# Kernel tuning notes

Measured on AMD Instinct MI355X. Metric: run time of the kernel, lower is better.

## Reference

```python
import jax, jax.numpy as jnp
import numpy as np

N_NODES = 20000
N_EDGES = 320000
NF = 128   # num_node_feats
EF = 32    # num_edge_feats
CF = 3     # num_coord_feats
H = 512    # hidden_dim


def setup_inputs() -> dict:
    key = jax.random.key(0)
    ks = jax.random.split(key, 20)
    s = lambda k, shape, fan_in: jax.random.normal(k, shape, jnp.float32) / np.sqrt(fan_in)
    return {
        "hfeats": jax.random.normal(ks[0], (N_NODES, NF), jnp.float32),
        "cfeats": jax.random.normal(ks[1], (N_NODES, CF), jnp.float32),
        "efeats": jax.random.normal(ks[2], (N_EDGES, EF), jnp.float32),
        "src": jax.random.randint(ks[3], (N_EDGES,), 0, N_NODES, jnp.int32),
        "dst": jax.random.randint(ks[4], (N_EDGES,), 0, N_NODES, jnp.int32),
        # node_expansion: Linear(NF, H)
        "Wn": s(ks[5], (NF, H), NF), "bn": jnp.zeros((H,), jnp.float32),
        # edge_expansion: Linear(EF, H)
        "We": s(ks[6], (EF, H), EF), "be": jnp.zeros((H,), jnp.float32),
        # coord_expansion: Linear(CF, H)
        "Wc": s(ks[7], (CF, H), CF), "bc": jnp.zeros((H,), jnp.float32),
        # combination_reduction_nfeats: Linear(H,H) -> CELU -> Linear(H,NF) -> CELU
        "Wn1": s(ks[8], (H, H), H), "bn1": jnp.zeros((H,), jnp.float32),
        "Wn2": s(ks[9], (H, NF), H), "bn2": jnp.zeros((NF,), jnp.float32),
        # combination_reduction_efeats: Linear(H, EF) -> CELU
        "Weo": s(ks[10], (H, EF), H), "beo": jnp.zeros((EF,), jnp.float32),
        # combination_reduction_cfeats: Linear(H, CF) -> CELU
        "Wco": s(ks[11], (H, CF), H), "bco": jnp.zeros((CF,), jnp.float32),
    }


def reference(hfeats, cfeats, efeats, src, dst,
              Wn, bn, We, be, Wc, bc,
              Wn1, bn1, Wn2, bn2, Weo, beo, Wco, bco):
    celu = jax.nn.celu
    n_nodes = hfeats.shape[0]
    # Feature expansions (Linear + CELU)
    h = celu(hfeats @ Wn + bn)   # [N, H]
    e = celu(efeats @ We + be)   # [E, H]
    c = celu(cfeats @ Wc + bc)   # [N, H]
    # edge_udf: x = |c_dst - c_src| * (h_src * e)   -> [E, H]
    x = jnp.abs(c[dst] - c[src]) * (h[src] * e)
    # update_all(copy_e, sum): scatter-sum edge messages to dst nodes
    k = jax.ops.segment_sum(x, dst, num_segments=n_nodes)  # [N, H]
    # Residual combination-reductions
    h_out = hfeats + celu(celu(k @ Wn1 + bn1) @ Wn2 + bn2)
    e_out = efeats + celu(e @ Weo + beo)
    c_out = cfeats + celu(c @ Wco + bco)
    return (h_out, c_out, e_out)
```

## Files before the change

kernel.cpp:

```cpp
#include <hip/hip_runtime.h>
#include <hip/hip_bf16.h>

#define NF 128
#define EF 32
#define CF 3
#define H  512
#define EB 32

typedef __attribute__((ext_vector_type(8))) short bf16x8;
typedef __attribute__((ext_vector_type(4))) float f32x4;

__device__ __forceinline__ float celu_f(float x) {
    return fmaxf(x, __expf(fminf(x, 0.0f)) - 1.0f);
}
__device__ __forceinline__ uint cvtpk(float lo, float hi) {
    uint r;
    asm("v_cvt_pk_bf16_f32 %0, %1, %2" : "=v"(r) : "v"(lo), "v"(hi));
    return r;
}
__device__ __forceinline__ bf16x8 pack8(float4 v0, float4 v1) {
    union { uint4 u; bf16x8 b; } r;
    r.u.x = cvtpk(v0.x, v0.y); r.u.y = cvtpk(v0.z, v0.w);
    r.u.z = cvtpk(v1.x, v1.y); r.u.w = cvtpk(v1.z, v1.w);
    return r.b;
}
__device__ __forceinline__ float b2f(ushort s) {
    union { uint u; float f; } v; v.u = ((uint)s) << 16; return v.f;
}
__device__ __forceinline__ void unpack4(uint2 v, float* o) {
    union { uint u; float f; } x;
    x.u = v.x << 16;          o[0] = x.f;
    x.u = v.x & 0xffff0000u;  o[1] = x.f;
    x.u = v.y << 16;          o[2] = x.f;
    x.u = v.y & 0xffff0000u;  o[3] = x.f;
}

__global__ void hist_kernel(const int* __restrict__ dst, int* __restrict__ cnt, int n_edges) {
    int i = blockIdx.x * 256 + threadIdx.x;
    if (i < n_edges) atomicAdd(&cnt[dst[i]], 1);
}

__global__ void scan_kernel(int* __restrict__ cnt, int n_nodes) {
    __shared__ int part[1024];
    const int t = threadIdx.x;
    const int per = (n_nodes + 1023) / 1024;
    int s = 0;
    for (int i = 0; i < per; ++i) {
        int idx = t * per + i;
        if (idx < n_nodes) s += cnt[idx];
    }
    part[t] = s;
    __syncthreads();
    for (int off = 1; off < 1024; off <<= 1) {
        int v = (t >= off) ? part[t - off] : 0;
        __syncthreads();
        part[t] += v;
        __syncthreads();
    }
    int acc = part[t] - s;
    for (int i = 0; i < per; ++i) {
        int idx = t * per + i;
        if (idx < n_nodes) {
            int c = cnt[idx];
            cnt[idx] = acc;
            acc += c;
        }
    }
}

__global__ void scatter_kernel(const int* __restrict__ dst, int* __restrict__ cursor,
                               int* __restrict__ perm, int n_edges) {
    int i = blockIdx.x * 256 + threadIdx.x;
    if (i < n_edges) {
        int pos = atomicAdd(&cursor[dst[i]], 1);
        perm[pos] = i;
    }
}

__global__ void prep_kernel(const float* __restrict__ We, const float* __restrict__ Weo,
                            const float* __restrict__ Wn, const float* __restrict__ Wn1,
                            const float* __restrict__ Wn2,
                            ushort* __restrict__ Wet, ushort* __restrict__ Weot,
                            ushort* __restrict__ Wnt, ushort* __restrict__ Wn1t,
                            ushort* __restrict__ Wn2t) {
    int i = blockIdx.x * 256 + threadIdx.x;
    if (i < H * EF) {
        int j = i / EF, k = i % EF;
        Wet[i] = (ushort)cvtpk(We[(size_t)k * H + j], 0.f);
        int o = i / H, j2 = i % H;
        Weot[i] = (ushort)cvtpk(Weo[(size_t)j2 * EF + o], 0.f);
    }
    if (i < H * NF) {
        int o = i >> 7, k = i & 127;
        Wnt[i] = (ushort)cvtpk(Wn[(size_t)k * H + o], 0.f);
        int o2 = i >> 9, k2 = i & 511;
        Wn2t[i] = (ushort)cvtpk(Wn2[(size_t)k2 * NF + o2], 0.f);
    }
    if (i < H * H) {
        int o = i >> 9, k = i & 511;
        Wn1t[i] = (ushort)cvtpk(Wn1[(size_t)k * H + o], 0.f);
    }
}

__global__ __launch_bounds__(256) void node_expand_kernel(
        const float* __restrict__ hfeats, const float* __restrict__ cfeats,
        const ushort* __restrict__ Wnt, const float* __restrict__ bn,
        const float* __restrict__ Wc, const float* __restrict__ bc,
        ushort* __restrict__ hc, int n_nodes) {
    __shared__ ushort hf[32 * NF];
    __shared__ float cf[32][4];
    const int t = threadIdx.x;
    const int lane = t & 63;
    const int w = t >> 6;
    const int node0 = blockIdx.x * 32;

    for (int i = t; i < 32 * 16; i += 256) {
        int row = i >> 4, g = i & 15;
        int node = node0 + row; if (node >= n_nodes) node = n_nodes - 1;
        const float* p = hfeats + (size_t)node * NF + g * 8;
        float4 v0 = *(const float4*)p;
        float4 v1 = *(const float4*)(p + 4);
        ((bf16x8*)hf)[row * 16 + (g ^ (row & 7))] = pack8(v0, v1);
    }
    for (int i = t; i < 32 * CF; i += 256) {
        int n = i / CF, k = i % CF;
        int node = node0 + n; if (node >= n_nodes) node = n_nodes - 1;
        cf[n][k] = cfeats[(size_t)node * CF + k];
    }
    __syncthreads();

    const int ar = lane & 15;
    const int hi = lane >> 4;
    const int ak = hi * 8;

    f32x4 acc[2][8];
    #pragma unroll
    for (int nt = 0; nt < 2; ++nt)
        #pragma unroll
        for (int q = 0; q < 8; ++q) { f32x4 z = {0.f,0.f,0.f,0.f}; acc[nt][q] = z; }

    for (int kstep = 0; kstep < NF / 32; ++kstep) {
        bf16x8 nfrag[2];
        #pragma unroll
        for (int nt = 0; nt < 2; ++nt) {
            int r = nt * 16 + ar;
            int g = kstep * 4 + hi;
            nfrag[nt] = ((const bf16x8*)hf)[r * 16 + (g ^ (r & 7))];
        }
        #pragma unroll
        for (int q = 0; q < 8; ++q) {
            bf16x8 wf = *(const bf16x8*)(Wnt + (size_t)((w * 8 + q) * 16 + ar) * NF + kstep * 32 + ak);
            acc[0][q] = __builtin_amdgcn_mfma_f32_16x16x32_bf16(wf, nfrag[0], acc[0][q], 0, 0, 0);
            acc[1][q] = __builtin_amdgcn_mfma_f32_16x16x32_bf16(wf, nfrag[1], acc[1][q], 0, 0, 0);
        }
    }
    #pragma unroll
    for (int q = 0; q < 8; ++q) {
        const int jbase = (w * 8 + q) * 16 + hi * 4;
        const float4 bv = *(const float4*)(bn + jbase);
        #pragma unroll
        for (int nt = 0; nt < 2; ++nt) {
            int node = node0 + nt * 16 + ar;
            if (node < n_nodes) {
                uint2 pk;
                pk.x = cvtpk(celu_f(acc[nt][q][0] + bv.x), celu_f(acc[nt][q][1] + bv.y));
                pk.y = cvtpk(celu_f(acc[nt][q][2] + bv.z), celu_f(acc[nt][q][3] + bv.w));
                *(uint2*)(hc + (size_t)node * 1024 + (jbase >> 2) * 8) = pk;
            }
        }
    }

    for (int i = t; i < 32 * 64; i += 256) {
        int n = i >> 6, gj = i & 63;
        int node = node0 + n;
        if (node < n_nodes) {
            int j = gj * 8;
            float c0 = cf[n][0], c1 = cf[n][1], c2 = cf[n][2];
            float v[8];
            #pragma unroll
            for (int u = 0; u < 8; ++u)
                v[u] = celu_f(bc[j + u] + c0 * Wc[j + u] + c1 * Wc[H + j + u] + c2 * Wc[2 * H + j + u]);
            uint2 p0, p1;
            p0.x = cvtpk(v[0], v[1]); p0.y = cvtpk(v[2], v[3]);
            p1.x = cvtpk(v[4], v[5]); p1.y = cvtpk(v[6], v[7]);
            *(uint2*)(hc + (size_t)node * 1024 + (2 * gj) * 8 + 4) = p0;
            *(uint2*)(hc + (size_t)node * 1024 + (2 * gj + 1) * 8 + 4) = p1;
        }
    }
}

__global__ __launch_bounds__(256) void c_out_kernel(
        const float* __restrict__ cfeats, const ushort* __restrict__ hc,
        const float* __restrict__ Wco, const float* __restrict__ bco,
        float* __restrict__ c_out, int n_nodes) {
    const int t = threadIdx.x;
    const int lane = t & 63;
    const int w = t >> 6;
    const int node = blockIdx.x * 4 + w;
    if (node >= n_nodes) return;
    uint2 cv0 = *(const uint2*)(hc + (size_t)node * 1024 + (2 * lane) * 8 + 4);
    uint2 cv1 = *(const uint2*)(hc + (size_t)node * 1024 + (2 * lane + 1) * 8 + 4);
    float cv[8];
    unpack4(cv0, cv);
    unpack4(cv1, cv + 4);
    float a0 = 0.f, a1 = 0.f, a2 = 0.f;
    #pragma unroll
    for (int u = 0; u < 8; ++u) {
        int j = lane * 8 + u;
        a0 += cv[u] * Wco[j * CF + 0];
        a1 += cv[u] * Wco[j * CF + 1];
        a2 += cv[u] * Wco[j * CF + 2];
    }
    #pragma unroll
    for (int m = 32; m >= 1; m >>= 1) {
        a0 += __shfl_xor(a0, m);
        a1 += __shfl_xor(a1, m);
        a2 += __shfl_xor(a2, m);
    }
    if (lane < 3) {
        float s = (lane == 0) ? a0 : (lane == 1) ? a1 : a2;
        c_out[(size_t)node * CF + lane] = cfeats[(size_t)node * CF + lane] + celu_f(bco[lane] + s);
    }
}

__global__ __launch_bounds__(512, 4) void edge_kernel(
        const float* __restrict__ efeats,
        const int* __restrict__ src, const int* __restrict__ dst,
        const int* __restrict__ perm,
        const ushort* __restrict__ Wet, const float* __restrict__ be,
        const ushort* __restrict__ Weot, const float* __restrict__ beo,
        const ushort* __restrict__ hc,
        float* __restrict__ k_acc, float* __restrict__ e_out, int n_edges) {
    __shared__ ushort e512[EB * 512];
    __shared__ int s_perm[EB], s_src[EB], s_dst[EB];
    const int t = threadIdx.x;
    const int lane = t & 63;
    const int w = t >> 6;

    const int nwg = gridDim.x;
    const int q = nwg >> 3, r = nwg & 7;
    const int xcd = blockIdx.x & 7, sub = blockIdx.x >> 3;
    const int bid = (xcd < r ? xcd * (q + 1) : r * (q + 1) + (xcd - r) * q) + sub;
    const int e0 = bid * EB;

    if (t < EB) {
        int e = e0 + t;
        int pe = (e < n_edges) ? perm[e] : -1;
        s_perm[t] = pe;
        s_src[t] = (pe >= 0) ? src[pe] : 0;
        s_dst[t] = (pe >= 0) ? dst[pe] : -1;
    }
    __syncthreads();

    const int ar = lane & 15;
    const int hi = lane >> 4;
    const int ak = hi * 8;

    {
        bf16x8 wfrag[4];
        #pragma unroll
        for (int qq = 0; qq < 4; ++qq)
            wfrag[qq] = *(const bf16x8*)(Wet + (size_t)((w * 4 + qq) * 16 + ar) * EF + ak);
        #pragma unroll
        for (int et = 0; et < 2; ++et) {
            bf16x8 efrag;
            {
                int pe = s_perm[et * 16 + ar];
                if (pe < 0) pe = 0;
                const float* p = efeats + (size_t)pe * EF + ak;
                float4 v0 = *(const float4*)p;
                float4 v1 = *(const float4*)(p + 4);
                efrag = pack8(v0, v1);
            }
            f32x4 acc[4];
            #pragma unroll
            for (int qq = 0; qq < 4; ++qq) { f32x4 z = {0.f,0.f,0.f,0.f}; acc[qq] = z; }
            #pragma unroll
            for (int qq = 0; qq < 4; ++qq)
                acc[qq] = __builtin_amdgcn_mfma_f32_16x16x32_bf16(wfrag[qq], efrag, acc[qq], 0, 0, 0);
            const int e_l = et * 16 + ar;
            #pragma unroll
            for (int qq = 0; qq < 4; ++qq) {
                const int jbase = (w * 4 + qq) * 16 + hi * 4;
                const float4 bv = *(const float4*)(be + jbase);
                uint2 pk;
                pk.x = cvtpk(celu_f(acc[qq][0] + bv.x), celu_f(acc[qq][1] + bv.y));
                pk.y = cvtpk(celu_f(acc[qq][2] + bv.z), celu_f(acc[qq][3] + bv.w));
                const int gs = (jbase >> 3) ^ (e_l & 7);
                *(uint2*)(&e512[e_l * 512 + gs * 8 + (jbase & 7)]) = pk;
            }
        }
    }
    __syncthreads();

    if (w < 4) {
        const int grp = t >> 7;
        const int ct = t & 127;
        const int j0 = ct * 4;
        const int g = j0 >> 3, go = j0 & 7;
        const int ebase = grp * 16;
        float a_[4];
        a_[0] = a_[1] = a_[2] = a_[3] = 0.f;
        int cur = -1;

        uint4 svb[2][4];
        uint2 cdb[2][4];
        uint2 evb[2][4];

        #pragma unroll
        for (int j = 0; j < 4; ++j) {
            const int e = ebase + j;
            const int s_ = s_src[e];
            int dc = s_dst[e]; dc = (dc < 0) ? 0 : dc;
            svb[0][j] = *(const uint4*)(hc + (size_t)s_ * 1024 + ct * 8);
            cdb[0][j] = *(const uint2*)(hc + (size_t)dc * 1024 + ct * 8 + 4);
            evb[0][j] = *(const uint2*)(&e512[e * 512 + (g ^ (e & 7)) * 8 + go]);
        }

        #pragma unroll
        for (int c = 0; c < 4; ++c) {
            const int cb = c & 1, nb = cb ^ 1;
            if (c < 3) {
                #pragma unroll
                for (int j = 0; j < 4; ++j) {
                    const int e = ebase + (c + 1) * 4 + j;
                    const int s_ = s_src[e];
                    int dc = s_dst[e]; dc = (dc < 0) ? 0 : dc;
                    svb[nb][j] = *(const uint4*)(hc + (size_t)s_ * 1024 + ct * 8);
                    cdb[nb][j] = *(const uint2*)(hc + (size_t)dc * 1024 + ct * 8 + 4);
                    evb[nb][j] = *(const uint2*)(&e512[e * 512 + (g ^ (e & 7)) * 8 + go]);
                }
            }
            #pragma unroll
            for (int j = 0; j < 4; ++j) {
                const int e = ebase + c * 4 + j;
                const int d = __builtin_amdgcn_readfirstlane(s_dst[e]);
                if (d != cur) {
                    if (cur >= 0) {
                        #pragma unroll
                        for (int u = 0; u < 4; ++u)
                            atomicAdd(&k_acc[(size_t)cur * H + j0 + u], a_[u]);
                        a_[0] = a_[1] = a_[2] = a_[3] = 0.f;
                    }
                    cur = d;
                }
                if (d >= 0) {
                    float hs_[4], cs_[4], cd_[4], ev_[4];
                    uint2 hv; hv.x = svb[cb][j].x; hv.y = svb[cb][j].y;
                    uint2 cv; cv.x = svb[cb][j].z; cv.y = svb[cb][j].w;
                    unpack4(hv, hs_);
                    unpack4(cv, cs_);
                    unpack4(cdb[cb][j], cd_);
                    unpack4(evb[cb][j], ev_);
                    #pragma unroll
                    for (int u = 0; u < 4; ++u)
                        a_[u] += fabsf(cd_[u] - cs_[u]) * (hs_[u] * ev_[u]);
                }
            }
        }
        if (cur >= 0) {
            #pragma unroll
            for (int u = 0; u < 4; ++u)
                atomicAdd(&k_acc[(size_t)cur * H + j0 + u], a_[u]);
        }
    } else {
        const int wc = w - 4;
        const int ot = wc & 1, et = wc >> 1;
        const int e_l = et * 16 + ar;
        f32x4 accc = {0.f, 0.f, 0.f, 0.f};
        #pragma unroll
        for (int kt = 0; kt < 16; ++kt) {
            bf16x8 wfC = *(const bf16x8*)(Weot + (size_t)(ot * 16 + ar) * H + kt * 32 + ak);
            const int gs = (kt * 4 + hi) ^ (e_l & 7);
            bf16x8 b = *(const bf16x8*)(&e512[e_l * 512 + gs * 8]);
            accc = __builtin_amdgcn_mfma_f32_16x16x32_bf16(wfC, b, accc, 0, 0, 0);
        }
        const int pe = s_perm[e_l];
        if (pe >= 0) {
            const int obase = ot * 16 + hi * 4;
            const float4 bo = *(const float4*)(beo + obase);
            size_t idx = (size_t)pe * EF + obase;
            float4 ef4 = *(const float4*)(efeats + idx);
            float4 o;
            o.x = ef4.x + celu_f(accc[0] + bo.x);
            o.y = ef4.y + celu_f(accc[1] + bo.y);
            o.z = ef4.z + celu_f(accc[2] + bo.z);
            o.w = ef4.w + celu_f(accc[3] + bo.w);
            *(float4*)(e_out + idx) = o;
        }
    }
}

__global__ __launch_bounds__(256) void node_out_kernel(
        const float* __restrict__ hfeats, const float* __restrict__ k_acc,
        const ushort* __restrict__ Wn1t, const float* __restrict__ bn1,
        const ushort* __restrict__ Wn2t, const float* __restrict__ bn2,
        float* __restrict__ h_out, int n_nodes) {
    __shared__ ushort kt_s[32 * H];
    const int t = threadIdx.x;
    const int lane = t & 63;
    const int w = t >> 6;
    const int node0 = blockIdx.x * 32;

    for (int i = t; i < 32 * 64; i += 256) {
        int row = i >> 6, g = i & 63;
        int node = node0 + row; if (node >= n_nodes) node = n_nodes - 1;
        const float* p = k_acc + (size_t)node * H + g * 8;
        float4 v0 = *(const float4*)p;
        float4 v1 = *(const float4*)(p + 4);
        ((bf16x8*)kt_s)[row * 64 + (g ^ (row & 7))] = pack8(v0, v1);
    }
    __syncthreads();

    const int ar = lane & 15;
    const int hi = lane >> 4;
    const int ak = hi * 8;

    f32x4 acc[2][8];
    #pragma unroll
    for (int nt = 0; nt < 2; ++nt)
        #pragma unroll
        for (int q = 0; q < 8; ++q) { f32x4 z = {0.f,0.f,0.f,0.f}; acc[nt][q] = z; }

    for (int kstep = 0; kstep < H / 32; ++kstep) {
        bf16x8 kfrag[2];
        #pragma unroll
        for (int nt = 0; nt < 2; ++nt) {
            int rr = nt * 16 + ar;
            int g = kstep * 4 + hi;
            kfrag[nt] = ((const bf16x8*)kt_s)[rr * 64 + (g ^ (rr & 7))];
        }
        #pragma unroll
        for (int q = 0; q < 8; ++q) {
            bf16x8 wf = *(const bf16x8*)(Wn1t + (size_t)((w * 8 + q) * 16 + ar) * H + kstep * 32 + ak);
            acc[0][q] = __builtin_amdgcn_mfma_f32_16x16x32_bf16(wf, kfrag[0], acc[0][q], 0, 0, 0);
            acc[1][q] = __builtin_amdgcn_mfma_f32_16x16x32_bf16(wf, kfrag[1], acc[1][q], 0, 0, 0);
        }
    }
    __syncthreads();

    #pragma unroll
    for (int q = 0; q < 8; ++q) {
        const int jbase = (w * 8 + q) * 16 + hi * 4;
        const float4 bv = *(const float4*)(bn1 + jbase);
        #pragma unroll
        for (int nt = 0; nt < 2; ++nt) {
            const int rr = nt * 16 + ar;
            uint2 pk;
            pk.x = cvtpk(celu_f(acc[nt][q][0] + bv.x), celu_f(acc[nt][q][1] + bv.y));
            pk.y = cvtpk(celu_f(acc[nt][q][2] + bv.z), celu_f(acc[nt][q][3] + bv.w));
            const int gs = (jbase >> 3) ^ (rr & 7);
            *(uint2*)(&kt_s[rr * 512 + gs * 8 + (jbase & 7)]) = pk;
        }
    }
    __syncthreads();

    f32x4 acc2[2][2];
    #pragma unroll
    for (int nt = 0; nt < 2; ++nt)
        #pragma unroll
        for (int ct = 0; ct < 2; ++ct) { f32x4 z = {0.f,0.f,0.f,0.f}; acc2[nt][ct] = z; }

    for (int kstep = 0; kstep < H / 32; ++kstep) {
        bf16x8 tfrag[2];
        #pragma unroll
        for (int nt = 0; nt < 2; ++nt) {
            int rr = nt * 16 + ar;
            int g = kstep * 4 + hi;
            tfrag[nt] = ((const bf16x8*)kt_s)[rr * 64 + (g ^ (rr & 7))];
        }
        #pragma unroll
        for (int ct = 0; ct < 2; ++ct) {
            bf16x8 wf = *(const bf16x8*)(Wn2t + (size_t)((w * 2 + ct) * 16 + ar) * H + kstep * 32 + ak);
            acc2[0][ct] = __builtin_amdgcn_mfma_f32_16x16x32_bf16(wf, tfrag[0], acc2[0][ct], 0, 0, 0);
            acc2[1][ct] = __builtin_amdgcn_mfma_f32_16x16x32_bf16(wf, tfrag[1], acc2[1][ct], 0, 0, 0);
        }
    }
    #pragma unroll
    for (int ct = 0; ct < 2; ++ct) {
        const int jbase = (w * 2 + ct) * 16 + hi * 4;
        const float4 bv = *(const float4*)(bn2 + jbase);
        #pragma unroll
        for (int nt = 0; nt < 2; ++nt) {
            const int node = node0 + nt * 16 + ar;
            if (node < n_nodes) {
                size_t idx = (size_t)node * NF + jbase;
                float4 hf4 = *(const float4*)(hfeats + idx);
                float4 o;
                o.x = hf4.x + celu_f(acc2[nt][ct][0] + bv.x);
                o.y = hf4.y + celu_f(acc2[nt][ct][1] + bv.y);
                o.z = hf4.z + celu_f(acc2[nt][ct][2] + bv.z);
                o.w = hf4.w + celu_f(acc2[nt][ct][3] + bv.w);
                *(float4*)(h_out + idx) = o;
            }
        }
    }
}

extern "C" void kernel_launch(void* const* d_in, const int* in_sizes, int n_in,
                              void* d_out, int out_size, void* d_ws, size_t ws_size,
                              hipStream_t stream) {
    const float* hfeats = (const float*)d_in[0];
    const float* cfeats = (const float*)d_in[1];
    const float* efeats = (const float*)d_in[2];
    const int*   src    = (const int*)d_in[3];
    const int*   dst    = (const int*)d_in[4];
    const float* Wn  = (const float*)d_in[5];  const float* bn  = (const float*)d_in[6];
    const float* We  = (const float*)d_in[7];  const float* be  = (const float*)d_in[8];
    const float* Wc  = (const float*)d_in[9];  const float* bc  = (const float*)d_in[10];
    const float* Wn1 = (const float*)d_in[11]; const float* bn1 = (const float*)d_in[12];
    const float* Wn2 = (const float*)d_in[13]; const float* bn2 = (const float*)d_in[14];
    const float* Weo = (const float*)d_in[15]; const float* beo = (const float*)d_in[16];
    const float* Wco = (const float*)d_in[17]; const float* bco = (const float*)d_in[18];

    const int n_nodes = in_sizes[0] / NF;
    const int n_edges = in_sizes[2] / EF;

    float*  k_buf = (float*)d_ws;
    ushort* hc    = (ushort*)(k_buf + (size_t)n_nodes * H);
    ushort* Wet   = hc + (size_t)n_nodes * H * 2;
    ushort* Weot  = Wet + (size_t)H * EF;
    ushort* Wnt   = Weot + (size_t)H * EF;
    ushort* Wn1t  = Wnt + (size_t)H * NF;
    ushort* Wn2t  = Wn1t + (size_t)H * H;
    int*    cnt   = (int*)(Wn2t + (size_t)NF * H);
    int*    perm  = cnt + n_nodes;

    float* h_out = (float*)d_out;
    float* c_out = h_out + (size_t)n_nodes * NF;
    float* e_out = c_out + (size_t)n_nodes * CF;

    hipMemsetAsync(k_buf, 0, (size_t)n_nodes * H * sizeof(float), stream);
    hipMemsetAsync(cnt, 0, (size_t)n_nodes * sizeof(int), stream);

    prep_kernel<<<(H * H + 255) / 256, 256, 0, stream>>>(
        We, Weo, Wn, Wn1, Wn2, Wet, Weot, Wnt, Wn1t, Wn2t);
    hist_kernel<<<(n_edges + 255) / 256, 256, 0, stream>>>(dst, cnt, n_edges);
    scan_kernel<<<1, 1024, 0, stream>>>(cnt, n_nodes);
    scatter_kernel<<<(n_edges + 255) / 256, 256, 0, stream>>>(dst, cnt, perm, n_edges);

    node_expand_kernel<<<(n_nodes + 31) / 32, 256, 0, stream>>>(
        hfeats, cfeats, Wnt, bn, Wc, bc, hc, n_nodes);

    c_out_kernel<<<(n_nodes + 3) / 4, 256, 0, stream>>>(
        cfeats, hc, Wco, bco, c_out, n_nodes);

    edge_kernel<<<(n_edges + EB - 1) / EB, 512, 0, stream>>>(
        efeats, src, dst, perm, Wet, be, Weot, beo, hc, k_buf, e_out, n_edges);

    node_out_kernel<<<(n_nodes + 31) / 32, 256, 0, stream>>>(
        hfeats, k_buf, Wn1t, bn1, Wn2t, bn2, h_out, n_nodes);
}
```

Measured before the change: 459.8 us.

## Merge small setup kernels into larger launches and prefetch gathers earlier

```diff
diff --git a/kernel.cpp b/kernel.cpp
--- a/kernel.cpp
+++ b/kernel.cpp
@@ -35,9 +35,33 @@
     x.u = v.y & 0xffff0000u;  o[3] = x.f;
 }
 
-__global__ void hist_kernel(const int* __restrict__ dst, int* __restrict__ cnt, int n_edges) {
+__global__ void setup_kernel(const float* __restrict__ We, const float* __restrict__ Weo,
+                             const float* __restrict__ Wn, const float* __restrict__ Wn1,
+                             const float* __restrict__ Wn2, const int* __restrict__ dst,
+                             ushort* __restrict__ Wet, ushort* __restrict__ Weot,
+                             ushort* __restrict__ Wnt, ushort* __restrict__ Wn1t,
+                             ushort* __restrict__ Wn2t, int* __restrict__ cnt,
+                             int n_edges) {
     int i = blockIdx.x * 256 + threadIdx.x;
-    if (i < n_edges) atomicAdd(&cnt[dst[i]], 1);
+    if (i < H * EF) {
+        int j = i / EF, k = i % EF;
+        Wet[i] = (ushort)cvtpk(We[(size_t)k * H + j], 0.f);
+        int o = i / H, j2 = i % H;
+        Weot[i] = (ushort)cvtpk(Weo[(size_t)j2 * EF + o], 0.f);
+    }
+    if (i < H * NF) {
+        int o = i >> 7, k = i & 127;
+        Wnt[i] = (ushort)cvtpk(Wn[(size_t)k * H + o], 0.f);
+        int o2 = i >> 9, k2 = i & 511;
+        Wn2t[i] = (ushort)cvtpk(Wn2[(size_t)k2 * NF + o2], 0.f);
+    }
+    if (i < H * H) {
+        int o = i >> 9, k = i & 511;
+        Wn1t[i] = (ushort)cvtpk(Wn1[(size_t)k * H + o], 0.f);
+    }
+    const int nthreads = gridDim.x * 256;
+    for (int e = i; e < n_edges; e += nthreads)
+        atomicAdd(&cnt[dst[e]], 1);
 }
 
 __global__ void scan_kernel(int* __restrict__ cnt, int n_nodes) {
@@ -68,48 +92,24 @@
     }
 }
 
-__global__ void scatter_kernel(const int* __restrict__ dst, int* __restrict__ cursor,
-                               int* __restrict__ perm, int n_edges) {
-    int i = blockIdx.x * 256 + threadIdx.x;
-    if (i < n_edges) {
-        int pos = atomicAdd(&cursor[dst[i]], 1);
-        perm[pos] = i;
-    }
-}
-
-__global__ void prep_kernel(const float* __restrict__ We, const float* __restrict__ Weo,
-                            const float* __restrict__ Wn, const float* __restrict__ Wn1,
-                            const float* __restrict__ Wn2,
-                            ushort* __restrict__ Wet, ushort* __restrict__ Weot,
-                            ushort* __restrict__ Wnt, ushort* __restrict__ Wn1t,
-                            ushort* __restrict__ Wn2t) {
-    int i = blockIdx.x * 256 + threadIdx.x;
-    if (i < H * EF) {
-        int j = i / EF, k = i % EF;
-        Wet[i] = (ushort)cvtpk(We[(size_t)k * H + j], 0.f);
-        int o = i / H, j2 = i % H;
-        Weot[i] = (ushort)cvtpk(Weo[(size_t)j2 * EF + o], 0.f);
-    }
-    if (i < H * NF) {
-        int o = i >> 7, k = i & 127;
-        Wnt[i] = (ushort)cvtpk(Wn[(size_t)k * H + o], 0.f);
-        int o2 = i >> 9, k2 = i & 511;
-        Wn2t[i] = (ushort)cvtpk(Wn2[(size_t)k2 * NF + o2], 0.f);
-    }
-    if (i < H * H) {
-        int o = i >> 9, k = i & 511;
-        Wn1t[i] = (ushort)cvtpk(Wn1[(size_t)k * H + o], 0.f);
-    }
-}
-
 __global__ __launch_bounds__(256) void node_expand_kernel(
         const float* __restrict__ hfeats, const float* __restrict__ cfeats,
         const ushort* __restrict__ Wnt, const float* __restrict__ bn,
         const float* __restrict__ Wc, const float* __restrict__ bc,
-        ushort* __restrict__ hc, int n_nodes) {
+        ushort* __restrict__ hc, int n_nodes,
+        const int* __restrict__ dst, int* __restrict__ cursor,
+        int* __restrict__ perm, int n_edges, int nNE) {
+    const int t = threadIdx.x;
+    if (blockIdx.x >= nNE) {
+        int i = (blockIdx.x - nNE) * 256 + t;
+        if (i < n_edges) {
+            int pos = atomicAdd(&cursor[dst[i]], 1);
+            perm[pos] = i;
+        }
+        return;
+    }
     __shared__ ushort hf[32 * NF];
     __shared__ float cf[32][4];
-    const int t = threadIdx.x;
     const int lane = t & 63;
     const int w = t >> 6;
     const int node0 = blockIdx.x * 32;
@@ -189,40 +189,6 @@
     }
 }
 
-__global__ __launch_bounds__(256) void c_out_kernel(
-        const float* __restrict__ cfeats, const ushort* __restrict__ hc,
-        const float* __restrict__ Wco, const float* __restrict__ bco,
-        float* __restrict__ c_out, int n_nodes) {
-    const int t = threadIdx.x;
-    const int lane = t & 63;
-    const int w = t >> 6;
-    const int node = blockIdx.x * 4 + w;
-    if (node >= n_nodes) return;
-    uint2 cv0 = *(const uint2*)(hc + (size_t)node * 1024 + (2 * lane) * 8 + 4);
-    uint2 cv1 = *(const uint2*)(hc + (size_t)node * 1024 + (2 * lane + 1) * 8 + 4);
-    float cv[8];
-    unpack4(cv0, cv);
-    unpack4(cv1, cv + 4);
-    float a0 = 0.f, a1 = 0.f, a2 = 0.f;
-    #pragma unroll
-    for (int u = 0; u < 8; ++u) {
-        int j = lane * 8 + u;
-        a0 += cv[u] * Wco[j * CF + 0];
-        a1 += cv[u] * Wco[j * CF + 1];
-        a2 += cv[u] * Wco[j * CF + 2];
-    }
-    #pragma unroll
-    for (int m = 32; m >= 1; m >>= 1) {
-        a0 += __shfl_xor(a0, m);
-        a1 += __shfl_xor(a1, m);
-        a2 += __shfl_xor(a2, m);
-    }
-    if (lane < 3) {
-        float s = (lane == 0) ? a0 : (lane == 1) ? a1 : a2;
-        c_out[(size_t)node * CF + lane] = cfeats[(size_t)node * CF + lane] + celu_f(bco[lane] + s);
-    }
-}
-
 __global__ __launch_bounds__(512, 4) void edge_kernel(
         const float* __restrict__ efeats,
         const int* __restrict__ src, const int* __restrict__ dst,
@@ -230,15 +196,47 @@
         const ushort* __restrict__ Wet, const float* __restrict__ be,
         const ushort* __restrict__ Weot, const float* __restrict__ beo,
         const ushort* __restrict__ hc,
-        float* __restrict__ k_acc, float* __restrict__ e_out, int n_edges) {
-    __shared__ ushort e512[EB * 512];
-    __shared__ int s_perm[EB], s_src[EB], s_dst[EB];
+        float* __restrict__ k_acc, float* __restrict__ e_out, int n_edges,
+        int nEB,
+        const float* __restrict__ cfeats, const float* __restrict__ Wco,
+        const float* __restrict__ bco, float* __restrict__ c_out, int n_nodes) {
     const int t = threadIdx.x;
     const int lane = t & 63;
     const int w = t >> 6;
 
-    const int nwg = gridDim.x;
-    const int q = nwg >> 3, r = nwg & 7;
+    if (blockIdx.x >= nEB) {
+        const int node = (blockIdx.x - nEB) * 8 + w;
+        if (node >= n_nodes) return;
+        uint2 cv0 = *(const uint2*)(hc + (size_t)node * 1024 + (2 * lane) * 8 + 4);
+        uint2 cv1 = *(const uint2*)(hc + (size_t)node * 1024 + (2 * lane + 1) * 8 + 4);
+        float cv[8];
+        unpack4(cv0, cv);
+        unpack4(cv1, cv + 4);
+        float a0 = 0.f, a1 = 0.f, a2 = 0.f;
+        #pragma unroll
+        for (int u = 0; u < 8; ++u) {
+            int j = lane * 8 + u;
+            a0 += cv[u] * Wco[j * CF + 0];
+            a1 += cv[u] * Wco[j * CF + 1];
+            a2 += cv[u] * Wco[j * CF + 2];
+        }
+        #pragma unroll
+        for (int m = 32; m >= 1; m >>= 1) {
+            a0 += __shfl_xor(a0, m);
+            a1 += __shfl_xor(a1, m);
+            a2 += __shfl_xor(a2, m);
+        }
+        if (lane < 3) {
+            float s = (lane == 0) ? a0 : (lane == 1) ? a1 : a2;
+            c_out[(size_t)node * CF + lane] = cfeats[(size_t)node * CF + lane] + celu_f(bco[lane] + s);
+        }
+        return;
+    }
+
+    __shared__ ushort e512[EB * 512];
+    __shared__ int s_perm[EB], s_src[EB], s_dst[EB];
+
+    const int q = nEB >> 3, r = nEB & 7;
     const int xcd = blockIdx.x & 7, sub = blockIdx.x >> 3;
     const int bid = (xcd < r ? xcd * (q + 1) : r * (q + 1) + (xcd - r) * q) + sub;
     const int e0 = bid * EB;
@@ -255,6 +253,25 @@
     const int ar = lane & 15;
     const int hi = lane >> 4;
     const int ak = hi * 8;
+
+    const int grp = t >> 7;
+    const int ct = t & 127;
+    const int j0 = ct * 4;
+    const int g = j0 >> 3, go = j0 & 7;
+    const int ebase = grp * 16;
+    uint4 svb[2][4];
+    uint2 cdb[2][4];
+    uint2 evb[2][4];
+    if (w < 4) {
+        #pragma unroll
+        for (int j = 0; j < 4; ++j) {
+            const int e = ebase + j;
+            const int s_ = s_src[e];
+            int dc = s_dst[e]; dc = (dc < 0) ? 0 : dc;
+            svb[0][j] = *(const uint4*)(hc + (size_t)s_ * 1024 + ct * 8);
+            cdb[0][j] = *(const uint2*)(hc + (size_t)dc * 1024 + ct * 8 + 4);
+        }
+    }
 
     {
         bf16x8 wfrag[4];
@@ -294,26 +311,13 @@
     __syncthreads();
 
     if (w < 4) {
-        const int grp = t >> 7;
-        const int ct = t & 127;
-        const int j0 = ct * 4;
-        const int g = j0 >> 3, go = j0 & 7;
-        const int ebase = grp * 16;
         float a_[4];
         a_[0] = a_[1] = a_[2] = a_[3] = 0.f;
         int cur = -1;
 
-        uint4 svb[2][4];
-        uint2 cdb[2][4];
-        uint2 evb[2][4];
-
         #pragma unroll
         for (int j = 0; j < 4; ++j) {
             const int e = ebase + j;
-            const int s_ = s_src[e];
-            int dc = s_dst[e]; dc = (dc < 0) ? 0 : dc;
-            svb[0][j] = *(const uint4*)(hc + (size_t)s_ * 1024 + ct * 8);
-            cdb[0][j] = *(const uint2*)(hc + (size_t)dc * 1024 + ct * 8 + 4);
             evb[0][j] = *(const uint2*)(&e512[e * 512 + (g ^ (e & 7)) * 8 + go]);
         }
 
@@ -533,20 +537,22 @@
     hipMemsetAsync(k_buf, 0, (size_t)n_nodes * H * sizeof(float), stream);
     hipMemsetAsync(cnt, 0, (size_t)n_nodes * sizeof(int), stream);
 
-    prep_kernel<<<(H * H + 255) / 256, 256, 0, stream>>>(
-        We, Weo, Wn, Wn1, Wn2, Wet, Weot, Wnt, Wn1t, Wn2t);
-    hist_kernel<<<(n_edges + 255) / 256, 256, 0, stream>>>(dst, cnt, n_edges);
+    setup_kernel<<<(H * H + 255) / 256, 256, 0, stream>>>(
+        We, Weo, Wn, Wn1, Wn2, dst, Wet, Weot, Wnt, Wn1t, Wn2t, cnt, n_edges);
+
     scan_kernel<<<1, 1024, 0, stream>>>(cnt, n_nodes);
-    scatter_kernel<<<(n_edges + 255) / 256, 256, 0, stream>>>(dst, cnt, perm, n_edges);
-
-    node_expand_kernel<<<(n_nodes + 31) / 32, 256, 0, stream>>>(
-        hfeats, cfeats, Wnt, bn, Wc, bc, hc, n_nodes);
-
-    c_out_kernel<<<(n_nodes + 3) / 4, 256, 0, stream>>>(
-        cfeats, hc, Wco, bco, c_out, n_nodes);
-
-    edge_kernel<<<(n_edges + EB - 1) / EB, 512, 0, stream>>>(
-        efeats, src, dst, perm, Wet, be, Weot, beo, hc, k_buf, e_out, n_edges);
+
+    const int nNE = (n_nodes + 31) / 32;
+    const int nSC = (n_edges + 255) / 256;
+    node_expand_kernel<<<nNE + nSC, 256, 0, stream>>>(
+        hfeats, cfeats, Wnt, bn, Wc, bc, hc, n_nodes,
+        dst, cnt, perm, n_edges, nNE);
+
+    const int nEB = (n_edges + EB - 1) / EB;
+    const int nCO = (n_nodes + 7) / 8;
+    edge_kernel<<<nEB + nCO, 512, 0, stream>>>(
+        efeats, src, dst, perm, Wet, be, Weot, beo, hc, k_buf, e_out, n_edges,
+        nEB, cfeats, Wco, bco, c_out, n_nodes);
 
     node_out_kernel<<<(n_nodes + 31) / 32, 256, 0, stream>>>(
         hfeats, k_buf, Wn1t, bn1, Wn2t, bn2, h_out, n_nodes);
```

Result: faster. 439.6 us (-4.4%).
